# Performance work log

Measured on AMD Instinct MI355X. Metric: run time of the kernel, lower is better.

The kernel has to match this reference:

```python
import jax, jax.numpy as jnp
import numpy as np

HEAD_SIZE = 64

def setup_inputs() -> dict:
    key = jax.random.key(0)
    k1, k2, k3, k4 = jax.random.split(key, 4)
    B, T, C = 4, 4096, 768
    s = 1.0 / np.sqrt(C)
    return {
        "x": jax.random.normal(k1, (B, T, C), dtype=jnp.float32),
        "Wq": jax.random.normal(k2, (C, HEAD_SIZE), dtype=jnp.float32) * s,
        "Wk": jax.random.normal(k3, (C, HEAD_SIZE), dtype=jnp.float32) * s,
        "Wv": jax.random.normal(k4, (C, HEAD_SIZE), dtype=jnp.float32) * s,
    }

def reference(x, Wq, Wk, Wv):
    # x: [B,T,C]; Wq/Wk/Wv: [C,H]
    T = x.shape[1]
    q = jnp.einsum('btc,ch->bth', x, Wq)
    k = jnp.einsum('btc,ch->bth', x, Wk)
    v = jnp.einsum('btc,ch->bth', x, Wv)
    scale = HEAD_SIZE ** (-0.5)
    wei = jnp.einsum('bth,bsh->bts', q, k) * scale  # [B,T,T]
    causal = jnp.tril(jnp.ones((T, T), dtype=bool))
    wei = jnp.where(causal, wei, -jnp.inf)
    wei = jax.nn.softmax(wei, axis=-1)
    # dropout p=0.0 -> identity
    out = jnp.einsum('bts,bsh->bth', wei, v)  # [B,T,H]
    return out
```

## Files before the change

### kernel.cpp

```cpp
#include <hip/hip_runtime.h>
#include <hip/hip_bf16.h>
#include <stdint.h>

typedef unsigned short u16;
typedef __attribute__((ext_vector_type(8))) __bf16 bf16x8;
typedef __attribute__((ext_vector_type(4))) float f32x4;

#define LOG2E 1.44269504088896340736f
#define FIXED_M 16.0f

__device__ inline u16 f2bf(float f){
  uint32_t u = __float_as_uint(f);
  u += 0x7FFFu + ((u >> 16) & 1u);
  return (u16)(u >> 16);
}
__device__ inline float bf2f(u16 v){
  return __uint_as_float(((uint32_t)v) << 16);
}

__global__ __launch_bounds__(256) void wt_kernel(const float* __restrict__ Wq,
                                                 const float* __restrict__ Wk,
                                                 const float* __restrict__ Wv,
                                                 u16* __restrict__ wtf){
  int idx = blockIdx.x * 256 + threadIdx.x;
  if (idx >= 192 * 768) return;
  int n = idx / 768, c = idx - n * 768;
  int h = n & 63;
  const float* W = (n < 64) ? Wq : ((n < 128) ? Wk : Wv);
  float v = W[c * 64 + h];
  if (n < 64) v *= 0.125f * LOG2E;
  int f = n >> 4, n16 = n & 15;
  int kstep = c >> 5, quad = (c >> 3) & 3, j = c & 7;
  wtf[(size_t)((f * 24 + kstep) * 64 + quad * 16 + n16) * 8 + j] = f2bf(v);
}

__global__ __launch_bounds__(256) void proj_kernel(const float* __restrict__ x,
                                                   const u16* __restrict__ wtf,
                                                   u16* __restrict__ qs,
                                                   u16* __restrict__ ks,
                                                   u16* __restrict__ vt){
  __shared__ float red[4][16][196];
  const int tid = threadIdx.x;
  const int w = tid >> 6, lane = tid & 63;
  const int n16 = lane & 15, quad = lane >> 4;
  const int rt = blockIdx.x * 16;
  const float* xr = x + (size_t)(rt + n16) * 768 + w * 192;

  const f32x4 fz = {0.f, 0.f, 0.f, 0.f};
  f32x4 acc[12];
#pragma unroll
  for (int f = 0; f < 12; ++f) acc[f] = fz;

#pragma unroll
  for (int kl = 0; kl < 6; ++kl){
    const float4 xa = *(const float4*)(xr + kl * 32 + quad * 8);
    const float4 xb = *(const float4*)(xr + kl * 32 + quad * 8 + 4);
    union { bf16x8 v; u16 e[8]; } ua;
    ua.e[0] = f2bf(xa.x); ua.e[1] = f2bf(xa.y);
    ua.e[2] = f2bf(xa.z); ua.e[3] = f2bf(xa.w);
    ua.e[4] = f2bf(xb.x); ua.e[5] = f2bf(xb.y);
    ua.e[6] = f2bf(xb.z); ua.e[7] = f2bf(xb.w);
#pragma unroll
    for (int f = 0; f < 12; ++f){
      bf16x8 bfrag = *(const bf16x8*)(wtf + (size_t)((f * 24 + w * 6 + kl) * 64 + lane) * 8);
      acc[f] = __builtin_amdgcn_mfma_f32_16x16x32_bf16(ua.v, bfrag, acc[f], 0, 0, 0);
    }
  }

#pragma unroll
  for (int f = 0; f < 12; ++f){
#pragma unroll
    for (int r = 0; r < 4; ++r)
      red[w][quad * 4 + r][f * 16 + n16] = acc[f][r];
  }
  __syncthreads();

  const int m = tid & 15, cg = tid >> 4;
  const int orow = rt + m;
  const int b = orow >> 12, t = orow & 4095;
#pragma unroll
  for (int i = 0; i < 12; ++i){
    int n = cg * 12 + i;
    float s = red[0][m][n] + red[1][m][n] + red[2][m][n] + red[3][m][n];
    u16 val = f2bf(s);
    if (n < 64)       qs[(size_t)orow * 64 + n]        = val;
    else if (n < 128) ks[(size_t)orow * 64 + (n - 64)] = val;
    else              vt[((size_t)b * 64 + (n - 128)) * 4096 + t] = val;
  }
}

__global__ __launch_bounds__(256) void flash_part(const u16* __restrict__ qs,
                                                  const u16* __restrict__ ks,
                                                  const u16* __restrict__ vtg,
                                                  u16* __restrict__ Opart,
                                                  float* __restrict__ ml){
  const int b  = blockIdx.x >> 8;
  const int qt = (blockIdx.x >> 2) & 63;
  const int ck = blockIdx.x & 3;
  const int kt0 = ck * 16;
  if (kt0 > qt) return;
  const int kt1 = min(qt, kt0 + 15);

  __shared__ u16 Ks[64 * 72];
  __shared__ u16 Vt[64 * 72];
  __shared__ u16 Ps[4 * 16 * 72];
  const int tid = threadIdx.x;
  const int w = tid >> 6, lane = tid & 63;
  const int n16 = lane & 15, quad = lane >> 4;
  const size_t bo = (size_t)b * 4096 * 64;
  const u16* qb = qs + bo;
  const u16* kb = ks + bo;
  const u16* vb = vtg + bo;

  const int qrow = qt * 64 + w * 16 + n16;
  bf16x8 qA0 = *(const bf16x8*)(qb + (size_t)qrow * 64 + quad * 8);
  bf16x8 qA1 = *(const bf16x8*)(qb + (size_t)qrow * 64 + 32 + quad * 8);

  const f32x4 fz = {0.f, 0.f, 0.f, 0.f};
  f32x4 O[4];
  float rs[4] = {0.f, 0.f, 0.f, 0.f};
#pragma unroll
  for (int f = 0; f < 4; ++f) O[f] = fz;

  const int c0r = tid >> 3,          c0p = tid & 7;
  const int c1r = (tid + 256) >> 3,  c1p = tid & 7;

  uint4 rk0 = *(const uint4*)(kb + (size_t)kt0 * 4096 + c0r * 64 + c0p * 8);
  uint4 rk1 = *(const uint4*)(kb + (size_t)kt0 * 4096 + c1r * 64 + c1p * 8);
  uint4 rv0 = *(const uint4*)(vb + (size_t)c0r * 4096 + kt0 * 64 + c0p * 8);
  uint4 rv1 = *(const uint4*)(vb + (size_t)c1r * 4096 + kt0 * 64 + c1p * 8);

  for (int kt = kt0; kt <= kt1; ++kt){
    *(uint4*)&Ks[c0r * 72 + c0p * 8] = rk0;
    *(uint4*)&Ks[c1r * 72 + c1p * 8] = rk1;
    *(uint4*)&Vt[c0r * 72 + c0p * 8] = rv0;
    *(uint4*)&Vt[c1r * 72 + c1p * 8] = rv1;
    __syncthreads();

    if (kt < kt1){
      rk0 = *(const uint4*)(kb + (size_t)(kt + 1) * 4096 + c0r * 64 + c0p * 8);
      rk1 = *(const uint4*)(kb + (size_t)(kt + 1) * 4096 + c1r * 64 + c1p * 8);
      rv0 = *(const uint4*)(vb + (size_t)c0r * 4096 + (kt + 1) * 64 + c0p * 8);
      rv1 = *(const uint4*)(vb + (size_t)c1r * 4096 + (kt + 1) * 64 + c1p * 8);
    }

    f32x4 S[4];
#pragma unroll
    for (int f = 0; f < 4; ++f){
      bf16x8 b0 = *(const bf16x8*)&Ks[(f * 16 + n16) * 72 + quad * 8];
      bf16x8 b1 = *(const bf16x8*)&Ks[(f * 16 + n16) * 72 + 32 + quad * 8];
      f32x4 s = fz;
      s = __builtin_amdgcn_mfma_f32_16x16x32_bf16(qA0, b0, s, 0, 0, 0);
      s = __builtin_amdgcn_mfma_f32_16x16x32_bf16(qA1, b1, s, 0, 0, 0);
      S[f] = s;
    }

    if (kt == qt){
#pragma unroll
      for (int f = 0; f < 4; ++f){
#pragma unroll
        for (int r = 0; r < 4; ++r){
          int col = kt * 64 + f * 16 + n16;
          int row = qt * 64 + w * 16 + quad * 4 + r;
          if (col > row) S[f][r] = -1e30f;
        }
      }
    }

#pragma unroll
    for (int f = 0; f < 4; ++f){
#pragma unroll
      for (int r = 0; r < 4; ++r){
        float p = __builtin_amdgcn_exp2f(S[f][r] - FIXED_M);
        S[f][r] = p;
        rs[r] += p;
      }
    }

#pragma unroll
    for (int f = 0; f < 4; ++f){
#pragma unroll
      for (int r = 0; r < 4; ++r)
        Ps[(w * 16 + quad * 4 + r) * 72 + f * 16 + n16] = f2bf(S[f][r]);
    }
    bf16x8 pA0 = *(const bf16x8*)&Ps[(w * 16 + n16) * 72 + quad * 8];
    bf16x8 pA1 = *(const bf16x8*)&Ps[(w * 16 + n16) * 72 + 32 + quad * 8];

#pragma unroll
    for (int f = 0; f < 4; ++f){
      bf16x8 v0 = *(const bf16x8*)&Vt[(f * 16 + n16) * 72 + quad * 8];
      bf16x8 v1 = *(const bf16x8*)&Vt[(f * 16 + n16) * 72 + 32 + quad * 8];
      O[f] = __builtin_amdgcn_mfma_f32_16x16x32_bf16(pA0, v0, O[f], 0, 0, 0);
      O[f] = __builtin_amdgcn_mfma_f32_16x16x32_bf16(pA1, v1, O[f], 0, 0, 0);
    }
    __syncthreads();
  }

#pragma unroll
  for (int r = 0; r < 4; ++r){
#pragma unroll
    for (int off = 1; off < 16; off <<= 1)
      rs[r] += __shfl_xor(rs[r], off, 16);
  }

  const size_t oidx = (size_t)blockIdx.x * 4096;
#pragma unroll
  for (int f = 0; f < 4; ++f){
#pragma unroll
    for (int r = 0; r < 4; ++r){
      int row_local = w * 16 + quad * 4 + r;
      Opart[oidx + (size_t)row_local * 64 + f * 16 + n16] = f2bf(O[f][r]);
    }
  }
  if (n16 == 0){
    float* lp = ml + (size_t)blockIdx.x * 64;
#pragma unroll
    for (int r = 0; r < 4; ++r)
      lp[w * 16 + quad * 4 + r] = rs[r];
  }
}

__global__ __launch_bounds__(256) void combine_kernel(const u16* __restrict__ Opart,
                                                      const float* __restrict__ ml,
                                                      float* __restrict__ out){
  const int bq = blockIdx.x;
  const int qt = bq & 63;
  const int nc = (qt >> 4) + 1;
  const int t = threadIdx.x;
  const int row = t >> 2, seg = t & 3;

  float L = 0.f;
  for (int c = 0; c < nc; ++c)
    L += ml[((size_t)bq * 4 + c) * 64 + row];
  const float invL = 1.0f / L;

  float acc[16];
#pragma unroll
  for (int j = 0; j < 16; ++j) acc[j] = 0.f;
  for (int c = 0; c < nc; ++c){
    const u16* p = Opart + ((size_t)bq * 4 + c) * 4096 + (size_t)row * 64 + seg * 16;
    uint4 d0 = *(const uint4*)p;
    uint4 d1 = *(const uint4*)(p + 8);
    const u16* e0 = (const u16*)&d0;
    const u16* e1 = (const u16*)&d1;
#pragma unroll
    for (int j = 0; j < 8; ++j){
      acc[j]     += bf2f(e0[j]);
      acc[8 + j] += bf2f(e1[j]);
    }
  }
  float* op = out + (size_t)bq * 4096 + (size_t)row * 64 + seg * 16;
#pragma unroll
  for (int j = 0; j < 4; ++j){
    float4 v = {acc[j*4] * invL, acc[j*4+1] * invL, acc[j*4+2] * invL, acc[j*4+3] * invL};
    *(float4*)(op + j * 4) = v;
  }
}

extern "C" void kernel_launch(void* const* d_in, const int* in_sizes, int n_in,
                              void* d_out, int out_size, void* d_ws, size_t ws_size,
                              hipStream_t stream){
  const float* x  = (const float*)d_in[0];
  const float* Wq = (const float*)d_in[1];
  const float* Wk = (const float*)d_in[2];
  const float* Wv = (const float*)d_in[3];
  float* out = (float*)d_out;

  u16* qs = (u16*)d_ws;
  u16* ks = qs + (size_t)16384 * 64;
  u16* vt = ks + (size_t)16384 * 64;
  u16* wtf = vt + (size_t)16384 * 64;
  u16* Opart = wtf + (size_t)192 * 768;
  float* ml = (float*)(Opart + (size_t)1024 * 4096);

  wt_kernel<<<576, 256, 0, stream>>>(Wq, Wk, Wv, wtf);
  proj_kernel<<<1024, 256, 0, stream>>>(x, wtf, qs, ks, vt);
  flash_part<<<1024, 256, 0, stream>>>(qs, ks, vt, Opart, ml);
  combine_kernel<<<256, 256, 0, stream>>>(Opart, ml, out);
}
```

Measured before the change: 149.5 us.

## Load K/V fragments directly from global into registers and split KV into 8 chunks

The flash kernel no longer stages K and V tiles through shared memory. Each lane loads its MFMA operand fragments straight from global memory (K prefetched one tile ahead, V loaded per tile), which removes the LDS writes and both block-wide barriers per iteration. The KV split goes from 4 to 8 chunks, doubling grid parallelism at the cost of more partial outputs, and the combine kernel is reworked into a flat per-thread 4-element reduction over 8 partials. Redundant global loads of K/V across the four waves now rely on cache hits instead of shared reuse, and the extra partial traffic adds combine work.

```diff
diff --git a/kernel.cpp b/kernel.cpp
--- a/kernel.cpp
+++ b/kernel.cpp
@@ -94,15 +94,13 @@
                                                   const u16* __restrict__ vtg,
                                                   u16* __restrict__ Opart,
                                                   float* __restrict__ ml){
-  const int b  = blockIdx.x >> 8;
-  const int qt = (blockIdx.x >> 2) & 63;
-  const int ck = blockIdx.x & 3;
-  const int kt0 = ck * 16;
+  const int b  = blockIdx.x >> 9;
+  const int qt = (blockIdx.x >> 3) & 63;
+  const int ck = blockIdx.x & 7;
+  const int kt0 = ck * 8;
   if (kt0 > qt) return;
-  const int kt1 = min(qt, kt0 + 15);
-
-  __shared__ u16 Ks[64 * 72];
-  __shared__ u16 Vt[64 * 72];
+  const int kt1 = min(qt, kt0 + 7);
+
   __shared__ u16 Ps[4 * 16 * 72];
   const int tid = threadIdx.x;
   const int w = tid >> 6, lane = tid & 63;
@@ -122,37 +120,43 @@
 #pragma unroll
   for (int f = 0; f < 4; ++f) O[f] = fz;
 
-  const int c0r = tid >> 3,          c0p = tid & 7;
-  const int c1r = (tid + 256) >> 3,  c1p = tid & 7;
-
-  uint4 rk0 = *(const uint4*)(kb + (size_t)kt0 * 4096 + c0r * 64 + c0p * 8);
-  uint4 rk1 = *(const uint4*)(kb + (size_t)kt0 * 4096 + c1r * 64 + c1p * 8);
-  uint4 rv0 = *(const uint4*)(vb + (size_t)c0r * 4096 + kt0 * 64 + c0p * 8);
-  uint4 rv1 = *(const uint4*)(vb + (size_t)c1r * 4096 + kt0 * 64 + c1p * 8);
+  const u16* kbase = kb + (size_t)kt0 * 4096 + (size_t)n16 * 64 + quad * 8;
+  const u16* vbase = vb + (size_t)n16 * 4096 + (size_t)kt0 * 64 + quad * 8;
+
+  bf16x8 k0[4], k1[4];
+#pragma unroll
+  for (int f = 0; f < 4; ++f){
+    k0[f] = *(const bf16x8*)(kbase + (size_t)f * 1024);
+    k1[f] = *(const bf16x8*)(kbase + (size_t)f * 1024 + 32);
+  }
 
   for (int kt = kt0; kt <= kt1; ++kt){
-    *(uint4*)&Ks[c0r * 72 + c0p * 8] = rk0;
-    *(uint4*)&Ks[c1r * 72 + c1p * 8] = rk1;
-    *(uint4*)&Vt[c0r * 72 + c0p * 8] = rv0;
-    *(uint4*)&Vt[c1r * 72 + c1p * 8] = rv1;
-    __syncthreads();
+    f32x4 S[4];
+#pragma unroll
+    for (int f = 0; f < 4; ++f){
+      f32x4 s = fz;
+      s = __builtin_amdgcn_mfma_f32_16x16x32_bf16(qA0, k0[f], s, 0, 0, 0);
+      s = __builtin_amdgcn_mfma_f32_16x16x32_bf16(qA1, k1[f], s, 0, 0, 0);
+      S[f] = s;
+    }
+
+    bf16x8 v0[4], v1[4];
+    {
+      const u16* vp = vbase + (size_t)(kt - kt0) * 64;
+#pragma unroll
+      for (int f = 0; f < 4; ++f){
+        v0[f] = *(const bf16x8*)(vp + (size_t)f * 65536);
+        v1[f] = *(const bf16x8*)(vp + (size_t)f * 65536 + 32);
+      }
+    }
 
     if (kt < kt1){
-      rk0 = *(const uint4*)(kb + (size_t)(kt + 1) * 4096 + c0r * 64 + c0p * 8);
-      rk1 = *(const uint4*)(kb + (size_t)(kt + 1) * 4096 + c1r * 64 + c1p * 8);
-      rv0 = *(const uint4*)(vb + (size_t)c0r * 4096 + (kt + 1) * 64 + c0p * 8);
-      rv1 = *(const uint4*)(vb + (size_t)c1r * 4096 + (kt + 1) * 64 + c1p * 8);
-    }
-
-    f32x4 S[4];
-#pragma unroll
-    for (int f = 0; f < 4; ++f){
-      bf16x8 b0 = *(const bf16x8*)&Ks[(f * 16 + n16) * 72 + quad * 8];
-      bf16x8 b1 = *(const bf16x8*)&Ks[(f * 16 + n16) * 72 + 32 + quad * 8];
-      f32x4 s = fz;
-      s = __builtin_amdgcn_mfma_f32_16x16x32_bf16(qA0, b0, s, 0, 0, 0);
-      s = __builtin_amdgcn_mfma_f32_16x16x32_bf16(qA1, b1, s, 0, 0, 0);
-      S[f] = s;
+      const u16* kp = kbase + (size_t)(kt - kt0 + 1) * 4096;
+#pragma unroll
+      for (int f = 0; f < 4; ++f){
+        k0[f] = *(const bf16x8*)(kp + (size_t)f * 1024);
+        k1[f] = *(const bf16x8*)(kp + (size_t)f * 1024 + 32);
+      }
     }
 
     if (kt == qt){
@@ -188,12 +192,9 @@
 
 #pragma unroll
     for (int f = 0; f < 4; ++f){
-      bf16x8 v0 = *(const bf16x8*)&Vt[(f * 16 + n16) * 72 + quad * 8];
-      bf16x8 v1 = *(const bf16x8*)&Vt[(f * 16 + n16) * 72 + 32 + quad * 8];
-      O[f] = __builtin_amdgcn_mfma_f32_16x16x32_bf16(pA0, v0, O[f], 0, 0, 0);
-      O[f] = __builtin_amdgcn_mfma_f32_16x16x32_bf16(pA1, v1, O[f], 0, 0, 0);
-    }
-    __syncthreads();
+      O[f] = __builtin_amdgcn_mfma_f32_16x16x32_bf16(pA0, v0[f], O[f], 0, 0, 0);
+      O[f] = __builtin_amdgcn_mfma_f32_16x16x32_bf16(pA1, v1[f], O[f], 0, 0, 0);
+    }
   }
 
 #pragma unroll
@@ -223,38 +224,28 @@
 __global__ __launch_bounds__(256) void combine_kernel(const u16* __restrict__ Opart,
                                                       const float* __restrict__ ml,
                                                       float* __restrict__ out){
-  const int bq = blockIdx.x;
+  const int gid = blockIdx.x * 256 + threadIdx.x;
+  const size_t base = (size_t)gid * 4;
+  const int bq = gid >> 10;
+  const int rem = (int)(base & 4095);
+  const int row = rem >> 6;
   const int qt = bq & 63;
-  const int nc = (qt >> 4) + 1;
-  const int t = threadIdx.x;
-  const int row = t >> 2, seg = t & 3;
+  const int nc = (qt >> 3) + 1;
 
   float L = 0.f;
-  for (int c = 0; c < nc; ++c)
-    L += ml[((size_t)bq * 4 + c) * 64 + row];
+  float a0 = 0.f, a1 = 0.f, a2 = 0.f, a3 = 0.f;
+  for (int c = 0; c < nc; ++c){
+    L += ml[((size_t)bq * 8 + c) * 64 + row];
+    const u16* p = Opart + ((size_t)bq * 8 + c) * 4096 + rem;
+    uint2 d = *(const uint2*)p;
+    a0 += bf2f((u16)(d.x & 0xffffu));
+    a1 += bf2f((u16)(d.x >> 16));
+    a2 += bf2f((u16)(d.y & 0xffffu));
+    a3 += bf2f((u16)(d.y >> 16));
+  }
   const float invL = 1.0f / L;
-
-  float acc[16];
-#pragma unroll
-  for (int j = 0; j < 16; ++j) acc[j] = 0.f;
-  for (int c = 0; c < nc; ++c){
-    const u16* p = Opart + ((size_t)bq * 4 + c) * 4096 + (size_t)row * 64 + seg * 16;
-    uint4 d0 = *(const uint4*)p;
-    uint4 d1 = *(const uint4*)(p + 8);
-    const u16* e0 = (const u16*)&d0;
-    const u16* e1 = (const u16*)&d1;
-#pragma unroll
-    for (int j = 0; j < 8; ++j){
-      acc[j]     += bf2f(e0[j]);
-      acc[8 + j] += bf2f(e1[j]);
-    }
-  }
-  float* op = out + (size_t)bq * 4096 + (size_t)row * 64 + seg * 16;
-#pragma unroll
-  for (int j = 0; j < 4; ++j){
-    float4 v = {acc[j*4] * invL, acc[j*4+1] * invL, acc[j*4+2] * invL, acc[j*4+3] * invL};
-    *(float4*)(op + j * 4) = v;
-  }
+  float4 v = {a0 * invL, a1 * invL, a2 * invL, a3 * invL};
+  *(float4*)(out + base) = v;
 }
 
 extern "C" void kernel_launch(void* const* d_in, const int* in_sizes, int n_in,
@@ -271,10 +262,10 @@
   u16* vt = ks + (size_t)16384 * 64;
   u16* wtf = vt + (size_t)16384 * 64;
   u16* Opart = wtf + (size_t)192 * 768;
-  float* ml = (float*)(Opart + (size_t)1024 * 4096);
+  float* ml = (float*)(Opart + (size_t)2048 * 4096);
 
   wt_kernel<<<576, 256, 0, stream>>>(Wq, Wk, Wv, wtf);
   proj_kernel<<<1024, 256, 0, stream>>>(x, wtf, qs, ks, vt);
-  flash_part<<<1024, 256, 0, stream>>>(qs, ks, vt, Opart, ml);
-  combine_kernel<<<256, 256, 0, stream>>>(Opart, ml, out);
-}
+  flash_part<<<2048, 256, 0, stream>>>(qs, ks, vt, Opart, ml);
+  combine_kernel<<<1024, 256, 0, stream>>>(Opart, ml, out);
+}
```

After: 236.1 us. 58.0% more time.
